# Kernel optimization log

Hardware: AMD Instinct MI355X
Metric: run time of the kernel (lower is better)

## Reference

```python
import jax, jax.numpy as jnp
from jax import lax
import numpy as np

# Config mirroring CSABlock(embed_dim=128, bs=8, heads=8, img_size=512, depth=2)
E = 128
BATCH = 8
HEADS = 8
RESO = 512 // 8      # 64
DEPTH = 2
SPLIT = 2            # split_size
C = 2 * E            # token dim = 256
C2 = C // 2          # per-branch dim
NH = HEADS // 2      # heads per branch
HID = 4 * C          # mlp hidden (mlp_ratio=4)
EPS = 1e-5


def setup_inputs() -> dict:
    key = jax.random.key(0)
    ks = iter(jax.random.split(key, 24))
    rn = lambda s, sd=0.02: jax.random.normal(next(ks), s, jnp.float32) * sd
    return {
        "x1": jax.random.normal(next(ks), (BATCH, E, RESO, RESO), jnp.float32),
        "x2": jax.random.normal(next(ks), (BATCH, E, RESO, RESO), jnp.float32),
        # conv_embed: Conv2d(C,C,3,1,1) + BatchNorm (eval) + LayerNorm
        "conv_w": rn((C, C, 3, 3)), "conv_b": jnp.zeros((C,), jnp.float32),
        "bn_g": jnp.ones((C,), jnp.float32), "bn_b": jnp.zeros((C,), jnp.float32),
        "bn_m": rn((C,), 0.1), "bn_v": jax.random.uniform(next(ks), (C,), jnp.float32) + 0.5,
        "ln0_g": jnp.ones((C,), jnp.float32), "ln0_b": jnp.zeros((C,), jnp.float32),
        # per-CSWinBlock params, stacked over DEPTH
        "n1_g": jnp.ones((DEPTH, C), jnp.float32), "n1_b": jnp.zeros((DEPTH, C), jnp.float32),
        "qkv_w": rn((DEPTH, C, 3 * C)),                       # Linear(dim, 3*dim, bias=False)
        "lepe_w": rn((DEPTH, 2, C2, 1, 3, 3)),                # depthwise get_v conv per branch
        "lepe_b": jnp.zeros((DEPTH, 2, C2), jnp.float32),
        "proj_w": rn((DEPTH, C, C)), "proj_b": jnp.zeros((DEPTH, C), jnp.float32),
        "n2_g": jnp.ones((DEPTH, C), jnp.float32), "n2_b": jnp.zeros((DEPTH, C), jnp.float32),
        "fc1_w": rn((DEPTH, C, HID)), "fc1_b": jnp.zeros((DEPTH, HID), jnp.float32),
        "fc2_w": rn((DEPTH, HID, C)), "fc2_b": jnp.zeros((DEPTH, C), jnp.float32),
    }


def _ln(x, g, b):
    mu = jnp.mean(x, -1, keepdims=True)
    var = jnp.mean((x - mu) ** 2, -1, keepdims=True)
    return (x - mu) * lax.rsqrt(var + EPS) * g + b


def _branch(q, k, v, Hs, Ws, dw_w, dw_b):
    """LePEAttention: cross-shaped stripe window attention with locally-enhanced PE.
    q,k,v: (B, L, C2); stripes of size Hs x Ws over a RESO x RESO grid."""
    B, L, c2 = q.shape
    H = W = RESO
    hd = c2 // NH
    scale = hd ** -0.5

    def to_win(t):  # (B,L,c2) -> (B*nW, NH, Hs*Ws, hd)
        t = t.reshape(B, H // Hs, Hs, W // Ws, Ws, c2)
        t = t.transpose(0, 1, 3, 2, 4, 5).reshape(-1, Hs * Ws, NH, hd)
        return t.transpose(0, 2, 1, 3)

    qw, kw = to_win(q), to_win(k)
    # v as per-window images for the depthwise LePE conv (padding is per-window)
    vimg = v.reshape(B, H // Hs, Hs, W // Ws, Ws, c2).transpose(0, 1, 3, 5, 2, 4)
    vimg = vimg.reshape(-1, c2, Hs, Ws)
    lepe = lax.conv_general_dilated(vimg, dw_w, (1, 1), [(1, 1), (1, 1)],
                                    dimension_numbers=("NCHW", "OIHW", "NCHW"),
                                    feature_group_count=c2) + dw_b[:, None, None]
    heads = lambda t: t.reshape(-1, NH, hd, Hs * Ws).transpose(0, 1, 3, 2)
    vw, lepe = heads(vimg), heads(lepe)

    attn = jax.nn.softmax(jnp.einsum("wnsd,wntd->wnst", qw * scale, kw), axis=-1)
    o = jnp.einsum("wnst,wntd->wnsd", attn, vw) + lepe      # (B*nW, NH, S, hd)
    # windows2img
    o = o.transpose(0, 2, 1, 3).reshape(B, H // Hs, W // Ws, Hs, Ws, c2)
    o = o.transpose(0, 1, 3, 2, 4, 5).reshape(B, L, c2)
    return o


def _forward(x1, x2, conv_w, conv_b, bn_g, bn_b, bn_m, bn_v, ln0_g, ln0_b,
             n1_g, n1_b, qkv_w, lepe_w, lepe_b, proj_w, proj_b,
             n2_g, n2_b, fc1_w, fc1_b, fc2_w, fc2_b):
    B, _, H, W = x1.shape
    t = jnp.concatenate([x1, x2], 1)                                   # (B, C, H, W)
    t = lax.conv_general_dilated(t, conv_w, (1, 1), [(1, 1), (1, 1)],
                                 dimension_numbers=("NCHW", "OIHW", "NCHW")) + conv_b[:, None, None]
    # BatchNorm2d in eval mode (running stats)
    t = (t - bn_m[:, None, None]) * lax.rsqrt(bn_v + EPS)[:, None, None] * bn_g[:, None, None] + bn_b[:, None, None]
    t = t.reshape(B, C, H * W).transpose(0, 2, 1)                      # b c h w -> b (h w) c
    t = _ln(t, ln0_g, ln0_b)

    for i in range(DEPTH):  # CSWinBlock x DEPTH
        img = _ln(t, n1_g[i], n1_b[i])
        qkv = (img @ qkv_w[i]).reshape(B, -1, 3, C)
        q, k, v = qkv[..., 0, :], qkv[..., 1, :], qkv[..., 2, :]
        # branch 0: horizontal stripes (H_sp=RESO, W_sp=SPLIT); branch 1: vertical
        xa = _branch(q[..., :C2], k[..., :C2], v[..., :C2], RESO, SPLIT, lepe_w[i, 0], lepe_b[i, 0])
        xb = _branch(q[..., C2:], k[..., C2:], v[..., C2:], SPLIT, RESO, lepe_w[i, 1], lepe_b[i, 1])
        att = jnp.concatenate([xa, xb], -1) @ proj_w[i] + proj_b[i]
        t = t + att
        y = _ln(t, n2_g[i], n2_b[i])
        t = t + (jax.nn.gelu(y @ fc1_w[i] + fc1_b[i], approximate=False) @ fc2_w[i] + fc2_b[i])

    x = t.transpose(0, 2, 1).reshape(B, C, H, W)
    return x[:, :E], x[:, E:]


def reference(x1, x2, conv_w, conv_b, bn_g, bn_b, bn_m, bn_v, ln0_g, ln0_b,
              n1_g, n1_b, qkv_w, lepe_w, lepe_b, proj_w, proj_b,
              n2_g, n2_b, fc1_w, fc1_b, fc2_w, fc2_b):
    return _forward(x1, x2, conv_w, conv_b, bn_g, bn_b, bn_m, bn_v, ln0_g, ln0_b,
                    n1_g, n1_b, qkv_w, lepe_w, lepe_b, proj_w, proj_b,
                    n2_g, n2_b, fc1_w, fc1_b, fc2_w, fc2_b)
```

## Files before the change

### kernel.cpp

```cpp
#include <hip/hip_runtime.h>
#include <hip/hip_bf16.h>

#define EPSV 1e-5f

using s8v = __attribute__((ext_vector_type(8))) short;
using f4v = __attribute__((ext_vector_type(4))) float;

__device__ __forceinline__ float bf2f(ushort u){
  union { unsigned int i; float f; } x; x.i = ((unsigned int)u)<<16; return x.f;
}
__device__ __forceinline__ ushort f2bf(float f){
  union { float f; unsigned int i; } x; x.f = f;
  unsigned int r = x.i + 0x7FFFu + ((x.i>>16)&1u);
  return (ushort)(r>>16);
}
__device__ __forceinline__ float wsum(float s){
  #pragma unroll
  for (int m=1;m<64;m<<=1) s += __shfl_xor(s, m);
  return s;
}

__device__ __forceinline__ void gload16(const void* g, void* l){
  __builtin_amdgcn_global_load_lds((__attribute__((address_space(1))) void*)g,
                                   (__attribute__((address_space(3))) void*)l, 16, 0, 0);
}

__global__ __launch_bounds__(256) void repack_in_k(const float* __restrict__ x1,
                                                   const float* __restrict__ x2,
                                                   ushort* __restrict__ Xin){
  __shared__ ushort tile[256][66];
  const int y = blockIdx.x, b = blockIdx.y, tid = threadIdx.x;
  const int xl = tid & 63, cq = tid >> 6;
  for (int it=0; it<64; it++){
    int ci = it*4 + cq;
    float v;
    if (ci < 128) v = x1[(((long)b*128 + ci)*64 + y)*64 + xl];
    else          v = x2[(((long)b*128 + (ci-128))*64 + y)*64 + xl];
    tile[ci][xl] = f2bf(v);
  }
  __syncthreads();
  for (int x=0; x<64; x++){
    Xin[(((long)b*66 + (y+1))*66 + (x+1))*256 + tid] = tile[tid][x];
  }
}

__global__ void repack_convw_k(const float* __restrict__ w, ushort* __restrict__ Wc){
  const long total = 256L*2304;
  for (long e = (long)blockIdx.x*blockDim.x + threadIdx.x; e < total; e += (long)gridDim.x*blockDim.x){
    int co = (int)(e / 2304), kk = (int)(e % 2304);
    int dd = kk >> 8, ci = kk & 255;
    Wc[e] = f2bf(w[((long)(co*256 + ci))*9 + dd]);
  }
}

__global__ void transpose_w_k(const float* __restrict__ src, ushort* __restrict__ dst, int K, int N){
  long total = (long)K*N;
  for (long e = (long)blockIdx.x*blockDim.x + threadIdx.x; e < total; e += (long)gridDim.x*blockDim.x){
    int k = (int)(e / N), n = (int)(e % N);
    dst[(long)n*K + k] = f2bf(src[e]);
  }
}

__global__ void bnprep_k(const float* cb, const float* g, const float* b,
                         const float* m, const float* v, float* sc, float* sh){
  int n = threadIdx.x;
  if (n < 256){
    float s = g[n] * rsqrtf(v[n] + EPSV);
    sc[n] = s;
    sh[n] = (cb[n] - m[n])*s + b[n];
  }
}

template<int EPI>
__global__ __launch_bounds__(256) void gemm_f(
    const ushort* __restrict__ A, const ushort* __restrict__ Xin,
    const ushort* __restrict__ Wt, const float* __restrict__ bias,
    const float* __restrict__ sc, const float* __restrict__ sh,
    float* __restrict__ T, const float* __restrict__ g1, const float* __restrict__ b1,
    const float* __restrict__ g2, const float* __restrict__ b2,
    ushort* __restrict__ Xb, float* __restrict__ dout, int K)
{
  constexpr bool CONVA = (EPI==0);
  __shared__ ushort SMEM[40960];
  const int tid = threadIdx.x, wid = tid>>6, lane = tid&63;
  const int m0 = blockIdx.x*64;
  const int l15 = lane&15, lg = lane>>4;
  const int rS = wid*8 + (lane>>3);
  const int cS = (((lane&7) ^ (lane>>3))*8);

  const ushort* pA[2];
  if (CONVA){
    #pragma unroll
    for (int j=0;j<2;j++){
      int t = m0 + j*32 + rS;
      int b = t>>12, y = (t>>6)&63, x = t&63;
      pA[j] = Xin + ((long)((b*66 + y+1)*66) + (x+1))*256 + cS;
    }
  } else {
    #pragma unroll
    for (int j=0;j<2;j++) pA[j] = A + (long)(m0 + j*32 + rS)*K + cS;
  }
  const ushort* pB[8];
  #pragma unroll
  for (int j=0;j<8;j++) pB[j] = Wt + (long)(j*32 + rS)*K + cS;

  auto stage = [&](int buf, int k0){
    ushort* AsB = SMEM + buf*20480;
    ushort* BsB = AsB + 4096;
    int koffA;
    if (CONVA){
      int dd = k0 >> 8;
      int dy = dd/3, dx = dd - dy*3;
      koffA = ((dy-1)*66 + (dx-1))*256 + (k0 & 255);
    } else koffA = k0;
    #pragma unroll
    for (int j=0;j<2;j++)
      gload16(pA[j] + koffA, (void*)&AsB[(j*256 + wid*64)*8]);
    #pragma unroll
    for (int j=0;j<8;j++)
      gload16(pB[j] + k0, (void*)&BsB[(j*256 + wid*64)*8]);
  };

  f4v acc[4][4] = {};

  int cur = 0;
  stage(0, 0);
  __syncthreads();
  for (int k0=0; k0<K; k0+=64){
    if (k0 + 64 < K) stage(cur^1, k0 + 64);
    const ushort* AsB = SMEM + cur*20480;
    const ushort* BsB = AsB + 4096;
    #pragma unroll
    for (int kk=0; kk<2; kk++){
      s8v a[4], b[4];
      const int kch = ((kk*4 + lg) ^ (l15 & 7))*8;
      #pragma unroll
      for (int mi=0;mi<4;mi++) a[mi] = *(const s8v*)&AsB[(mi*16 + l15)*64 + kch];
      #pragma unroll
      for (int ni=0;ni<4;ni++) b[ni] = *(const s8v*)&BsB[(wid*64 + ni*16 + l15)*64 + kch];
      #pragma unroll
      for (int mi=0;mi<4;mi++)
        #pragma unroll
        for (int ni=0;ni<4;ni++)
          acc[mi][ni] = __builtin_amdgcn_mfma_f32_16x16x32_bf16(a[mi], b[ni], acc[mi][ni], 0,0,0);
    }
    __syncthreads();
    cur ^= 1;
  }

  float* CT = (float*)SMEM;
  #pragma unroll
  for (int mi=0;mi<4;mi++)
    #pragma unroll
    for (int ni=0;ni<4;ni++)
      #pragma unroll
      for (int r=0;r<4;r++)
        CT[(mi*16 + lg*4 + r)*256 + wid*64 + ni*16 + l15] = acc[mi][ni][r];
  __syncthreads();

  const int c0 = lane*4;
  float4 scv4, shv4, bias4, g1v, b1v, g2v, b2v;
  if (EPI==0){
    scv4 = *(const float4*)&sc[c0]; shv4 = *(const float4*)&sh[c0];
    g1v = *(const float4*)&g1[c0];  b1v = *(const float4*)&b1[c0];
    g2v = *(const float4*)&g2[c0];  b2v = *(const float4*)&b2[c0];
  } else {
    bias4 = *(const float4*)&bias[c0];
    if (EPI==1){ g1v = *(const float4*)&g1[c0]; b1v = *(const float4*)&b1[c0]; }
  }

  for (int t=0; t<16; t++){
    const int r = wid*16 + t;
    const long gmr = m0 + r;
    float4 v = *(float4*)&CT[r*256 + c0];
    float4 t4;
    if (EPI==0){
      t4.x = v.x*scv4.x + shv4.x; t4.y = v.y*scv4.y + shv4.y;
      t4.z = v.z*scv4.z + shv4.z; t4.w = v.w*scv4.w + shv4.w;
    } else {
      float4 rv = *(float4*)&T[gmr*256 + c0];
      t4.x = rv.x + v.x + bias4.x; t4.y = rv.y + v.y + bias4.y;
      t4.z = rv.z + v.z + bias4.z; t4.w = rv.w + v.w + bias4.w;
    }
    if (EPI==3){
      *(float4*)&CT[r*256 + c0] = t4;
    } else {
      float mu = wsum(t4.x+t4.y+t4.z+t4.w) * (1.0f/256.0f);
      float d0=t4.x-mu, d1=t4.y-mu, d2=t4.z-mu, d3=t4.w-mu;
      float rs = rsqrtf(wsum(d0*d0+d1*d1+d2*d2+d3*d3)*(1.0f/256.0f) + EPSV);
      if (EPI==0){
        float u0 = d0*rs*g1v.x + b1v.x, u1 = d1*rs*g1v.y + b1v.y;
        float u2 = d2*rs*g1v.z + b1v.z, u3 = d3*rs*g1v.w + b1v.w;
        float4 u = {u0,u1,u2,u3};
        *(float4*)&T[gmr*256 + c0] = u;
        float mu2 = wsum(u0+u1+u2+u3) * (1.0f/256.0f);
        float e0=u0-mu2, e1=u1-mu2, e2=u2-mu2, e3=u3-mu2;
        float rs2 = rsqrtf(wsum(e0*e0+e1*e1+e2*e2+e3*e3)*(1.0f/256.0f) + EPSV);
        ushort4 o; o.x=f2bf(e0*rs2*g2v.x + b2v.x); o.y=f2bf(e1*rs2*g2v.y + b2v.y);
        o.z=f2bf(e2*rs2*g2v.z + b2v.z); o.w=f2bf(e3*rs2*g2v.w + b2v.w);
        *(ushort4*)&Xb[gmr*256 + c0] = o;
      } else {
        *(float4*)&T[gmr*256 + c0] = t4;
        ushort4 o; o.x=f2bf(d0*rs*g1v.x + b1v.x); o.y=f2bf(d1*rs*g1v.y + b1v.y);
        o.z=f2bf(d2*rs*g1v.z + b1v.z); o.w=f2bf(d3*rs*g1v.w + b1v.w);
        *(ushort4*)&Xb[gmr*256 + c0] = o;
      }
    }
  }

  if (EPI==3){
    __syncthreads();
    const int b_ = m0>>12, y_ = (m0>>6)&63;
    float* obase = dout + (long)b_*524288 + (long)y_*64;
    for (int it=0; it<64; it++){
      int e = it*256 + tid;
      int c = e>>6, x = e&63;
      obase[(long)(c>>7)*4194304 + (long)(c&127)*4096 + x] = CT[x*256 + c];
    }
  }
}

#define BM 128
#define BN 128
#define BK 64
template<int EPI>
__global__ __launch_bounds__(256) void gemm_k(
    const ushort* __restrict__ A,
    const ushort* __restrict__ Wt, const float* __restrict__ bias,
    ushort* __restrict__ outb, int N, int K)
{
  __shared__ ushort SMEM[BM*BK + BN*BK];
  ushort* As = SMEM;
  ushort* Bs = SMEM + BM*BK;
  const int tid = threadIdx.x, wid = tid>>6, lane = tid&63;
  const int m0 = blockIdx.x*BM, n0 = blockIdx.y*BN;
  const int wm = (wid>>1)*64, wn = (wid&1)*64;
  const int l15 = lane&15, lg = lane>>4;

  const int rA = wid*32 + (lane>>3);
  const int cS = (((lane&7) ^ (lane>>3))*8);
  const ushort* pA[4];
  #pragma unroll
  for (int j=0;j<4;j++) pA[j] = A + (long)(m0 + rA + j*8)*K + cS;
  const ushort* pB[4];
  #pragma unroll
  for (int j=0;j<4;j++) pB[j] = Wt + (long)(n0 + rA + j*8)*K + cS;

  f4v acc[4][4] = {};

  for (int k0=0; k0<K; k0+=BK){
    #pragma unroll
    for (int j=0;j<4;j++){
      gload16(pA[j] + k0, (void*)&As[(wid*32 + j*8)*BK]);
      gload16(pB[j] + k0, (void*)&Bs[(wid*32 + j*8)*BK]);
    }
    __syncthreads();
    #pragma unroll
    for (int kk=0; kk<2; kk++){
      s8v a[4], b[4];
      const int kch = ((kk*4 + lg) ^ (l15 & 7))*8;
      #pragma unroll
      for (int mi=0;mi<4;mi++) a[mi] = *(const s8v*)&As[(wm + mi*16 + l15)*BK + kch];
      #pragma unroll
      for (int ni=0;ni<4;ni++) b[ni] = *(const s8v*)&Bs[(wn + ni*16 + l15)*BK + kch];
      #pragma unroll
      for (int mi=0;mi<4;mi++)
        #pragma unroll
        for (int ni=0;ni<4;ni++)
          acc[mi][ni] = __builtin_amdgcn_mfma_f32_16x16x32_bf16(a[mi], b[ni], acc[mi][ni], 0,0,0);
    }
    __syncthreads();
  }

  if (EPI == 4){
    #pragma unroll
    for (int mi=0;mi<4;mi++)
      #pragma unroll
      for (int ni=0;ni<4;ni++)
        #pragma unroll
        for (int r=0;r<4;r++){
          int gm = m0 + wm + mi*16 + lg*4 + r;
          int gn = n0 + wn + ni*16 + l15;
          float v = acc[mi][ni][r];
          int tile = gn >> 8;
          int c = gn & 255;
          int br2 = (c >> 7) & 1;
          int hh = (c >> 5) & 3;
          int d = c & 31;
          int bb2 = gm >> 12;
          int y = (gm >> 6) & 63;
          int x = gm & 63;
          int wv, sv;
          if (br2 == 0){ wv = x >> 1; sv = (y << 1) | (x & 1); }
          else         { wv = y >> 1; sv = ((y & 1) << 6) | x; }
          long row = ((long)bb2*32 + wv)*128 + sv;
          outb[(((long)(tile*2 + br2)*4 + hh)*32768L + row)*32 + d] = f2bf(v);
        }
  } else {
    float* CT = (float*)SMEM;
    #pragma unroll
    for (int p=0; p<2; p++){
      if ((wid>>1) == p){
        #pragma unroll
        for (int mi=0;mi<4;mi++)
          #pragma unroll
          for (int ni=0;ni<4;ni++)
            #pragma unroll
            for (int r=0;r<4;r++)
              CT[(mi*16 + lg*4 + r)*128 + wn + ni*16 + l15] = acc[mi][ni][r];
      }
      __syncthreads();
      #pragma unroll
      for (int it=0; it<8; it++){
        int e = it*256 + tid;
        int row = e >> 5;
        int c4 = e & 31;
        float4 v = *(float4*)&CT[row*128 + c4*4];
        int gm = m0 + p*64 + row;
        int gn = n0 + c4*4;
        float4 bv = *(const float4*)&bias[gn];
        float t0 = v.x + bv.x, t1 = v.y + bv.y, t2 = v.z + bv.z, t3 = v.w + bv.w;
        t0 = 0.5f*t0*(1.0f + erff(t0*0.70710678118654752f));
        t1 = 0.5f*t1*(1.0f + erff(t1*0.70710678118654752f));
        t2 = 0.5f*t2*(1.0f + erff(t2*0.70710678118654752f));
        t3 = 0.5f*t3*(1.0f + erff(t3*0.70710678118654752f));
        ushort4 u; u.x=f2bf(t0); u.y=f2bf(t1); u.z=f2bf(t2); u.w=f2bf(t3);
        *(ushort4*)&outb[(long)gm*N + gn] = u;
      }
      __syncthreads();
    }
  }
}

template<int BR>
__global__ __launch_bounds__(256) void attn_k(
    const ushort* __restrict__ QKVw, ushort* __restrict__ ATT,
    const float* __restrict__ lepe_w, const float* __restrict__ lepe_b, int layer)
{
  __shared__ ushort q_lds[128][36];
  __shared__ ushort k_lds[128][36];
  __shared__ ushort vT[32][132];
  __shared__ float wl[32][9];
  __shared__ float bl[32];
  const int tid = threadIdx.x, wid = tid>>6, lane = tid&63;
  const int b = blockIdx.y;
  const int w = blockIdx.x>>2, h = blockIdx.x&3;
  const int choff = BR*128 + h*32;
  const int l15 = lane&15, lg = lane>>4;

  const long rowbase = ((long)b*32 + w)*128;
  const ushort* qb = QKVw + (((long)(0*2+BR)*4 + h)*32768L + rowbase)*32;
  const ushort* kb = QKVw + (((long)(1*2+BR)*4 + h)*32768L + rowbase)*32;
  const ushort* vb = QKVw + (((long)(2*2+BR)*4 + h)*32768L + rowbase)*32;

  for (int e = tid; e < 512; e += 256){
    int row = e>>2, c4 = (e&3)*8;
    *(uint4*)&q_lds[row][c4] = *(const uint4*)(qb + (long)e*8);
    *(uint4*)&k_lds[row][c4] = *(const uint4*)(kb + (long)e*8);
    uint4 val = *(const uint4*)(vb + (long)e*8);
    const ushort* u = (const ushort*)&val;
    #pragma unroll
    for (int jj=0;jj<8;jj++) vT[c4+jj][row] = u[jj];
  }
  for (int e = tid; e < 288; e += 256){
    int d = e/9, tap = e%9;
    wl[d][tap] = lepe_w[((long)((layer*2+BR)*128 + h*32 + d))*9 + tap];
  }
  if (tid < 32) bl[tid] = lepe_b[(layer*2+BR)*128 + h*32 + tid];
  __syncthreads();

  const int wrow = wid*32;
  const float scale = 0.17677669529663689f;
  const int srcE = (lane & 15) | ((lane & 16) << 1);
  const int srcO = srcE + 16;
  const bool hi = (lane >= 32);

  #pragma unroll
  for (int mi=0; mi<2; mi++){
    s8v aq = *(const s8v*)&q_lds[wrow + mi*16 + l15][lg*8];
    f4v S[8];
    #pragma unroll
    for (int ni=0; ni<8; ni++){
      s8v bk = *(const s8v*)&k_lds[ni*16 + l15][lg*8];
      f4v z = {0.f,0.f,0.f,0.f};
      S[ni] = __builtin_amdgcn_mfma_f32_16x16x32_bf16(bk, aq, z, 0,0,0);
    }
    float mx = -1e30f;
    #pragma unroll
    for (int ni=0; ni<8; ni++)
      #pragma unroll
      for (int r=0;r<4;r++){ S[ni][r] *= scale; mx = fmaxf(mx, S[ni][r]); }
    mx = fmaxf(mx, __shfl_xor(mx, 16));
    mx = fmaxf(mx, __shfl_xor(mx, 32));
    float sum = 0.f;
    #pragma unroll
    for (int ni=0; ni<8; ni++)
      #pragma unroll
      for (int r=0;r<4;r++){ S[ni][r] = __expf(S[ni][r]-mx); sum += S[ni][r]; }
    sum += __shfl_xor(sum, 16);
    sum += __shfl_xor(sum, 32);
    const float inv = 1.0f / sum;
    unsigned int Alo[8], Ahi[8];
    #pragma unroll
    for (int ni=0; ni<8; ni++){
      Alo[ni] = (unsigned)f2bf(S[ni][0]*inv) | ((unsigned)f2bf(S[ni][1]*inv)<<16);
      Ahi[ni] = (unsigned)f2bf(S[ni][2]*inv) | ((unsigned)f2bf(S[ni][3]*inv)<<16);
    }
    f4v acc2[2] = {{0.f,0.f,0.f,0.f},{0.f,0.f,0.f,0.f}};
    #pragma unroll
    for (int ks=0; ks<4; ks++){
      unsigned e0 = (unsigned)__shfl((int)Alo[2*ks],   srcE);
      unsigned e1 = (unsigned)__shfl((int)Ahi[2*ks],   srcE);
      unsigned e2 = (unsigned)__shfl((int)Alo[2*ks+1], srcE);
      unsigned e3 = (unsigned)__shfl((int)Ahi[2*ks+1], srcE);
      unsigned o0 = (unsigned)__shfl((int)Alo[2*ks],   srcO);
      unsigned o1 = (unsigned)__shfl((int)Ahi[2*ks],   srcO);
      unsigned o2 = (unsigned)__shfl((int)Alo[2*ks+1], srcO);
      unsigned o3 = (unsigned)__shfl((int)Ahi[2*ks+1], srcO);
      union { unsigned u[4]; s8v v; } ap;
      ap.u[0] = hi?e2:e0; ap.u[1] = hi?e3:e1; ap.u[2] = hi?o2:o0; ap.u[3] = hi?o3:o1;
      #pragma unroll
      for (int di=0; di<2; di++){
        s8v bv = *(const s8v*)&vT[di*16 + l15][ks*32 + lg*8];
        acc2[di] = __builtin_amdgcn_mfma_f32_16x16x32_bf16(ap.v, bv, acc2[di], 0,0,0);
      }
    }
    #pragma unroll
    for (int di=0; di<2; di++)
      #pragma unroll
      for (int r=0;r<4;r++){
        int s = wrow + mi*16 + lg*4 + r;
        int d = di*16 + l15;
        float v = acc2[di][r] + bl[d];
        const int HsL = (BR==0)?64:2, WsL = (BR==0)?2:64;
        int hs, ws2;
        if (BR==0){ hs = s>>1; ws2 = s&1; }
        else      { hs = s>>6; ws2 = s&63; }
        #pragma unroll
        for (int a=-1;a<=1;a++)
          #pragma unroll
          for (int bb=-1;bb<=1;bb++){
            int h2 = hs+a, w2 = ws2+bb;
            if (h2>=0 && h2<HsL && w2>=0 && w2<WsL){
              int s2 = h2*WsL + w2;
              v += wl[d][(a+1)*3 + (bb+1)] * bf2f(vT[d][s2]);
            }
          }
        int y, x;
        if (BR==0){ y = s>>1; x = (w<<1)|(s&1); }
        else      { y = (w<<1)|(s>>6); x = s&63; }
        long tok = ((long)b*64 + y)*64 + x;
        ATT[tok*256 + choff + d] = f2bf(v);
      }
  }
}

extern "C" void kernel_launch(void* const* d_in, const int* in_sizes, int n_in,
                              void* d_out, int out_size, void* d_ws, size_t ws_size,
                              hipStream_t stream)
{
  (void)in_sizes; (void)n_in; (void)out_size;
  const float* x1     = (const float*)d_in[0];
  const float* x2     = (const float*)d_in[1];
  const float* conv_w = (const float*)d_in[2];
  const float* conv_b = (const float*)d_in[3];
  const float* bn_g   = (const float*)d_in[4];
  const float* bn_b   = (const float*)d_in[5];
  const float* bn_m   = (const float*)d_in[6];
  const float* bn_v   = (const float*)d_in[7];
  const float* ln0_g  = (const float*)d_in[8];
  const float* ln0_b  = (const float*)d_in[9];
  const float* n1_g   = (const float*)d_in[10];
  const float* n1_b   = (const float*)d_in[11];
  const float* qkv_w  = (const float*)d_in[12];
  const float* lepe_w = (const float*)d_in[13];
  const float* lepe_b = (const float*)d_in[14];
  const float* proj_w = (const float*)d_in[15];
  const float* proj_b = (const float*)d_in[16];
  const float* n2_g   = (const float*)d_in[17];
  const float* n2_b   = (const float*)d_in[18];
  const float* fc1_w  = (const float*)d_in[19];
  const float* fc1_b  = (const float*)d_in[20];
  const float* fc2_w  = (const float*)d_in[21];
  const float* fc2_b  = (const float*)d_in[22];

  if (ws_size < 121767936ULL){
    hipMemsetAsync(d_out, 0, (size_t)out_size*4, stream);
    return;
  }

  char* ws = (char*)d_ws;
  ushort* Xin  = (ushort*)ws;
  ushort* QKVb = (ushort*)ws;
  ushort* H1b  = (ushort*)ws;
  ushort* ATTb = (ushort*)(ws + 50331648);
  float*  T    = (float*)(ws + 67108864);
  ushort* Xb   = (ushort*)(ws + 100663296);
  size_t off = 117440512;
  ushort* Wc   = (ushort*)(ws + off); off += 1179648;
  ushort* Wq   = (ushort*)(ws + off); off += 786432;
  ushort* Wp   = (ushort*)(ws + off); off += 262144;
  ushort* W1   = (ushort*)(ws + off); off += 1048576;
  ushort* W2   = (ushort*)(ws + off); off += 1048576;
  float*  scv  = (float*)(ws + off);  off += 1024;
  float*  shv  = (float*)(ws + off);  off += 1024;

  hipMemsetAsync(Xin, 0, (size_t)8*66*66*256*2, stream);
  repack_in_k<<<dim3(64,8), 256, 0, stream>>>(x1, x2, Xin);
  repack_convw_k<<<576, 256, 0, stream>>>(conv_w, Wc);
  for (int i=0;i<2;i++){
    transpose_w_k<<<512,256,0,stream>>>(qkv_w + (long)i*196608, Wq + (long)i*196608, 256, 768);
    transpose_w_k<<<128,256,0,stream>>>(proj_w + (long)i*65536, Wp + (long)i*65536, 256, 256);
    transpose_w_k<<<512,256,0,stream>>>(fc1_w + (long)i*262144, W1 + (long)i*262144, 256, 1024);
    transpose_w_k<<<512,256,0,stream>>>(fc2_w + (long)i*262144, W2 + (long)i*262144, 1024, 256);
  }
  bnprep_k<<<1,256,0,stream>>>(conv_b, bn_g, bn_b, bn_m, bn_v, scv, shv);

  gemm_f<0><<<512,256,0,stream>>>(nullptr, Xin, Wc, nullptr, scv, shv,
                                  T, ln0_g, ln0_b, n1_g, n1_b, Xb, nullptr, 2304);

  for (int i=0;i<2;i++){
    gemm_k<4><<<dim3(256,6),256,0,stream>>>(Xb, Wq + (long)i*196608, nullptr, QKVb, 768, 256);
    attn_k<0><<<dim3(128,8),256,0,stream>>>(QKVb, ATTb, lepe_w, lepe_b, i);
    attn_k<1><<<dim3(128,8),256,0,stream>>>(QKVb, ATTb, lepe_w, lepe_b, i);
    gemm_f<1><<<512,256,0,stream>>>(ATTb, nullptr, Wp + (long)i*65536, proj_b + i*256,
                                    nullptr, nullptr, T, n2_g + i*256, n2_b + i*256,
                                    nullptr, nullptr, Xb, nullptr, 256);
    gemm_k<1><<<dim3(256,8),256,0,stream>>>(Xb, W1 + (long)i*262144, fc1_b + i*1024, H1b, 1024, 256);
    if (i == 0){
      gemm_f<1><<<512,256,0,stream>>>(H1b, nullptr, W2, fc2_b,
                                      nullptr, nullptr, T, n1_g + 256, n1_b + 256,
                                      nullptr, nullptr, Xb, nullptr, 1024);
    } else {
      gemm_f<3><<<512,256,0,stream>>>(H1b, nullptr, W2 + 262144, fc2_b + 256,
                                      nullptr, nullptr, T, nullptr, nullptr,
                                      nullptr, nullptr, nullptr, (float*)d_out, 1024);
    }
  }
}
```

Before: 486.5 us.

## Fuse MLP fc1, GELU and fc2 into one kernel; stage QKV epilogue through LDS

Adds an mlp_f kernel. Each block computes a 64-row fc1 tile in chunks of 256 hidden units, applies bias and GELU, and keeps the bf16 hidden tile in swizzled LDS. It then accumulates fc2 directly and finishes with the residual add and LayerNorm or the final output transpose. This removes the global write and re-read of the 1024-wide hidden activation each layer, at the cost of re-streaming both weight matrices per block from L2. It also uses more LDS per block and has no double buffering. Separately, the QKV GEMM epilogue now stages bf16 results in swizzled LDS and writes coalesced 16-byte segments into the stripe layout, replacing scattered per-element stores.

Measured after the change: 549.3 us. 1.13x slower.

```diff
diff --git a/kernel.cpp b/kernel.cpp
--- a/kernel.cpp
+++ b/kernel.cpp
@@ -18,6 +18,9 @@
   #pragma unroll
   for (int m=1;m<64;m<<=1) s += __shfl_xor(s, m);
   return s;
+}
+__device__ __forceinline__ float gelu_f(float t){
+  return 0.5f*t*(1.0f + erff(t*0.70710678118654752f));
 }
 
 __device__ __forceinline__ void gload16(const void* g, void* l){
@@ -166,7 +169,7 @@
     g2v = *(const float4*)&g2[c0];  b2v = *(const float4*)&b2[c0];
   } else {
     bias4 = *(const float4*)&bias[c0];
-    if (EPI==1){ g1v = *(const float4*)&g1[c0]; b1v = *(const float4*)&b1[c0]; }
+    g1v = *(const float4*)&g1[c0]; b1v = *(const float4*)&b1[c0];
   }
 
   for (int t=0; t<16; t++){
@@ -182,29 +185,149 @@
       t4.x = rv.x + v.x + bias4.x; t4.y = rv.y + v.y + bias4.y;
       t4.z = rv.z + v.z + bias4.z; t4.w = rv.w + v.w + bias4.w;
     }
+    float mu = wsum(t4.x+t4.y+t4.z+t4.w) * (1.0f/256.0f);
+    float d0=t4.x-mu, d1=t4.y-mu, d2=t4.z-mu, d3=t4.w-mu;
+    float rs = rsqrtf(wsum(d0*d0+d1*d1+d2*d2+d3*d3)*(1.0f/256.0f) + EPSV);
+    if (EPI==0){
+      float u0 = d0*rs*g1v.x + b1v.x, u1 = d1*rs*g1v.y + b1v.y;
+      float u2 = d2*rs*g1v.z + b1v.z, u3 = d3*rs*g1v.w + b1v.w;
+      float4 u = {u0,u1,u2,u3};
+      *(float4*)&T[gmr*256 + c0] = u;
+      float mu2 = wsum(u0+u1+u2+u3) * (1.0f/256.0f);
+      float e0=u0-mu2, e1=u1-mu2, e2=u2-mu2, e3=u3-mu2;
+      float rs2 = rsqrtf(wsum(e0*e0+e1*e1+e2*e2+e3*e3)*(1.0f/256.0f) + EPSV);
+      ushort4 o; o.x=f2bf(e0*rs2*g2v.x + b2v.x); o.y=f2bf(e1*rs2*g2v.y + b2v.y);
+      o.z=f2bf(e2*rs2*g2v.z + b2v.z); o.w=f2bf(e3*rs2*g2v.w + b2v.w);
+      *(ushort4*)&Xb[gmr*256 + c0] = o;
+    } else {
+      *(float4*)&T[gmr*256 + c0] = t4;
+      ushort4 o; o.x=f2bf(d0*rs*g1v.x + b1v.x); o.y=f2bf(d1*rs*g1v.y + b1v.y);
+      o.z=f2bf(d2*rs*g1v.z + b1v.z); o.w=f2bf(d3*rs*g1v.w + b1v.w);
+      *(ushort4*)&Xb[gmr*256 + c0] = o;
+    }
+  }
+}
+
+template<int EPI>
+__global__ __launch_bounds__(256) void mlp_f(
+    const ushort* __restrict__ Xb, const ushort* __restrict__ W1t, const float* __restrict__ w1b,
+    const ushort* __restrict__ W2t, const float* __restrict__ w2b,
+    float* __restrict__ T, const float* __restrict__ lng, const float* __restrict__ lnb,
+    ushort* __restrict__ XbOut, float* __restrict__ dout)
+{
+  __shared__ ushort SMEM[36864];
+  ushort* As = SMEM;
+  ushort* Bs = SMEM + 4096;
+  ushort* H  = SMEM + 20480;
+  const int tid = threadIdx.x, wid = tid>>6, lane = tid&63;
+  const int m0 = blockIdx.x*64;
+  const int l15 = lane&15, lg = lane>>4;
+  const int rS = wid*8 + (lane>>3);
+  const int cS = (((lane&7) ^ (lane>>3))*8);
+
+  const ushort* pA[2];
+  #pragma unroll
+  for (int j=0;j<2;j++) pA[j] = Xb + (long)(m0 + j*32 + rS)*256 + cS;
+
+  f4v acc2[4][4] = {};
+
+  for (int hc=0; hc<4; hc++){
+    f4v acc1[4][4] = {};
+    for (int ks=0; ks<4; ks++){
+      const int k0 = ks*64;
+      #pragma unroll
+      for (int j=0;j<2;j++)
+        gload16(pA[j] + k0, (void*)&As[(j*256 + wid*64)*8]);
+      #pragma unroll
+      for (int j=0;j<8;j++)
+        gload16(W1t + (long)(hc*256 + j*32 + rS)*256 + k0 + cS, (void*)&Bs[(j*256 + wid*64)*8]);
+      __syncthreads();
+      #pragma unroll
+      for (int kk=0; kk<2; kk++){
+        s8v a[4], b[4];
+        const int kch = ((kk*4 + lg) ^ (l15 & 7))*8;
+        #pragma unroll
+        for (int mi=0;mi<4;mi++) a[mi] = *(const s8v*)&As[(mi*16 + l15)*64 + kch];
+        #pragma unroll
+        for (int ni=0;ni<4;ni++) b[ni] = *(const s8v*)&Bs[(wid*64 + ni*16 + l15)*64 + kch];
+        #pragma unroll
+        for (int mi=0;mi<4;mi++)
+          #pragma unroll
+          for (int ni=0;ni<4;ni++)
+            acc1[mi][ni] = __builtin_amdgcn_mfma_f32_16x16x32_bf16(a[mi], b[ni], acc1[mi][ni], 0,0,0);
+      }
+      __syncthreads();
+    }
+    #pragma unroll
+    for (int ni=0;ni<4;ni++){
+      const int c = wid*64 + ni*16 + l15;
+      const float bv = w1b[hc*256 + c];
+      const int j = c>>3, ce = c&7;
+      #pragma unroll
+      for (int mi=0;mi<4;mi++)
+        #pragma unroll
+        for (int r=0;r<4;r++){
+          const int row = mi*16 + lg*4 + r;
+          H[row*256 + (((j ^ (row&7))<<3) | ce)] = f2bf(gelu_f(acc1[mi][ni][r] + bv));
+        }
+    }
+    for (int ks2=0; ks2<4; ks2++){
+      #pragma unroll
+      for (int j=0;j<8;j++)
+        gload16(W2t + (long)(j*32 + rS)*1024 + hc*256 + ks2*64 + cS, (void*)&Bs[(j*256 + wid*64)*8]);
+      __syncthreads();
+      #pragma unroll
+      for (int kk=0; kk<2; kk++){
+        s8v a[4], b[4];
+        const int kch = ((kk*4 + lg) ^ (l15 & 7))*8;
+        #pragma unroll
+        for (int mi=0;mi<4;mi++)
+          a[mi] = *(const s8v*)&H[(mi*16 + l15)*256 + (((ks2*8 + kk*4 + lg) ^ (l15&7))*8)];
+        #pragma unroll
+        for (int ni=0;ni<4;ni++) b[ni] = *(const s8v*)&Bs[(wid*64 + ni*16 + l15)*64 + kch];
+        #pragma unroll
+        for (int mi=0;mi<4;mi++)
+          #pragma unroll
+          for (int ni=0;ni<4;ni++)
+            acc2[mi][ni] = __builtin_amdgcn_mfma_f32_16x16x32_bf16(a[mi], b[ni], acc2[mi][ni], 0,0,0);
+      }
+      __syncthreads();
+    }
+  }
+
+  float* CT = (float*)SMEM;
+  #pragma unroll
+  for (int mi=0;mi<4;mi++)
+    #pragma unroll
+    for (int ni=0;ni<4;ni++)
+      #pragma unroll
+      for (int r=0;r<4;r++)
+        CT[(mi*16 + lg*4 + r)*256 + wid*64 + ni*16 + l15] = acc2[mi][ni][r];
+  __syncthreads();
+
+  const int c0 = lane*4;
+  const float4 bias4 = *(const float4*)&w2b[c0];
+  float4 g1v, b1v;
+  if (EPI==1){ g1v = *(const float4*)&lng[c0]; b1v = *(const float4*)&lnb[c0]; }
+
+  for (int t=0; t<16; t++){
+    const int r = wid*16 + t;
+    const long gmr = m0 + r;
+    float4 v = *(float4*)&CT[r*256 + c0];
+    float4 rv = *(float4*)&T[gmr*256 + c0];
+    float4 t4;
+    t4.x = rv.x + v.x + bias4.x; t4.y = rv.y + v.y + bias4.y;
+    t4.z = rv.z + v.z + bias4.z; t4.w = rv.w + v.w + bias4.w;
     if (EPI==3){
       *(float4*)&CT[r*256 + c0] = t4;
     } else {
+      *(float4*)&T[gmr*256 + c0] = t4;
       float mu = wsum(t4.x+t4.y+t4.z+t4.w) * (1.0f/256.0f);
       float d0=t4.x-mu, d1=t4.y-mu, d2=t4.z-mu, d3=t4.w-mu;
       float rs = rsqrtf(wsum(d0*d0+d1*d1+d2*d2+d3*d3)*(1.0f/256.0f) + EPSV);
-      if (EPI==0){
-        float u0 = d0*rs*g1v.x + b1v.x, u1 = d1*rs*g1v.y + b1v.y;
-        float u2 = d2*rs*g1v.z + b1v.z, u3 = d3*rs*g1v.w + b1v.w;
-        float4 u = {u0,u1,u2,u3};
-        *(float4*)&T[gmr*256 + c0] = u;
-        float mu2 = wsum(u0+u1+u2+u3) * (1.0f/256.0f);
-        float e0=u0-mu2, e1=u1-mu2, e2=u2-mu2, e3=u3-mu2;
-        float rs2 = rsqrtf(wsum(e0*e0+e1*e1+e2*e2+e3*e3)*(1.0f/256.0f) + EPSV);
-        ushort4 o; o.x=f2bf(e0*rs2*g2v.x + b2v.x); o.y=f2bf(e1*rs2*g2v.y + b2v.y);
-        o.z=f2bf(e2*rs2*g2v.z + b2v.z); o.w=f2bf(e3*rs2*g2v.w + b2v.w);
-        *(ushort4*)&Xb[gmr*256 + c0] = o;
-      } else {
-        *(float4*)&T[gmr*256 + c0] = t4;
-        ushort4 o; o.x=f2bf(d0*rs*g1v.x + b1v.x); o.y=f2bf(d1*rs*g1v.y + b1v.y);
-        o.z=f2bf(d2*rs*g1v.z + b1v.z); o.w=f2bf(d3*rs*g1v.w + b1v.w);
-        *(ushort4*)&Xb[gmr*256 + c0] = o;
-      }
+      ushort4 o; o.x=f2bf(d0*rs*g1v.x + b1v.x); o.y=f2bf(d1*rs*g1v.y + b1v.y);
+      o.z=f2bf(d2*rs*g1v.z + b1v.z); o.w=f2bf(d3*rs*g1v.w + b1v.w);
+      *(ushort4*)&XbOut[gmr*256 + c0] = o;
     }
   }
 
@@ -223,11 +346,10 @@
 #define BM 128
 #define BN 128
 #define BK 64
-template<int EPI>
-__global__ __launch_bounds__(256) void gemm_k(
+__global__ __launch_bounds__(256) void gemm_qkv(
     const ushort* __restrict__ A,
-    const ushort* __restrict__ Wt, const float* __restrict__ bias,
-    ushort* __restrict__ outb, int N, int K)
+    const ushort* __restrict__ Wt,
+    ushort* __restrict__ outb, int K)
 {
   __shared__ ushort SMEM[BM*BK + BN*BK];
   ushort* As = SMEM;
@@ -272,62 +394,48 @@
     __syncthreads();
   }
 
-  if (EPI == 4){
+  ushort* CB = SMEM;
+  #pragma unroll
+  for (int ni=0;ni<4;ni++){
+    const int c = wn + ni*16 + l15;
+    const int j = c>>3, ce = c&7;
     #pragma unroll
     for (int mi=0;mi<4;mi++)
       #pragma unroll
-      for (int ni=0;ni<4;ni++)
-        #pragma unroll
-        for (int r=0;r<4;r++){
-          int gm = m0 + wm + mi*16 + lg*4 + r;
-          int gn = n0 + wn + ni*16 + l15;
-          float v = acc[mi][ni][r];
-          int tile = gn >> 8;
-          int c = gn & 255;
-          int br2 = (c >> 7) & 1;
-          int hh = (c >> 5) & 3;
-          int d = c & 31;
-          int bb2 = gm >> 12;
-          int y = (gm >> 6) & 63;
-          int x = gm & 63;
-          int wv, sv;
-          if (br2 == 0){ wv = x >> 1; sv = (y << 1) | (x & 1); }
-          else         { wv = y >> 1; sv = ((y & 1) << 6) | x; }
-          long row = ((long)bb2*32 + wv)*128 + sv;
-          outb[(((long)(tile*2 + br2)*4 + hh)*32768L + row)*32 + d] = f2bf(v);
-        }
+      for (int r=0;r<4;r++){
+        const int row = wm + mi*16 + lg*4 + r;
+        CB[row*128 + (((j ^ (row&7))<<3) | ce)] = f2bf(acc[mi][ni][r]);
+      }
+  }
+  __syncthreads();
+
+  const int tile = n0 >> 8;
+  const int brq  = (n0 >> 7) & 1;
+  const int b_   = m0 >> 12;
+  const int Y0   = (m0 >> 6) & 63;
+  if (brq == 0){
+    #pragma unroll
+    for (int it=0; it<8; it++){
+      int g = it*256 + tid;
+      int seg = g >> 4, q = g & 15;
+      int h = seg >> 5, wv = seg & 31;
+      int svi = q >> 2, c8 = q & 3;
+      int gm_local = (svi>>1)*64 + wv*2 + (svi&1);
+      int jc = h*4 + c8;
+      uint4 v = *(uint4*)&CB[gm_local*128 + ((jc ^ (gm_local&7))<<3)];
+      long rowb = ((long)(tile*2)*4 + h)*32768L + ((long)b_*32 + wv)*128 + (Y0*2 + svi);
+      *(uint4*)&outb[rowb*32 + c8*8] = v;
+    }
   } else {
-    float* CT = (float*)SMEM;
-    #pragma unroll
-    for (int p=0; p<2; p++){
-      if ((wid>>1) == p){
-        #pragma unroll
-        for (int mi=0;mi<4;mi++)
-          #pragma unroll
-          for (int ni=0;ni<4;ni++)
-            #pragma unroll
-            for (int r=0;r<4;r++)
-              CT[(mi*16 + lg*4 + r)*128 + wn + ni*16 + l15] = acc[mi][ni][r];
-      }
-      __syncthreads();
-      #pragma unroll
-      for (int it=0; it<8; it++){
-        int e = it*256 + tid;
-        int row = e >> 5;
-        int c4 = e & 31;
-        float4 v = *(float4*)&CT[row*128 + c4*4];
-        int gm = m0 + p*64 + row;
-        int gn = n0 + c4*4;
-        float4 bv = *(const float4*)&bias[gn];
-        float t0 = v.x + bv.x, t1 = v.y + bv.y, t2 = v.z + bv.z, t3 = v.w + bv.w;
-        t0 = 0.5f*t0*(1.0f + erff(t0*0.70710678118654752f));
-        t1 = 0.5f*t1*(1.0f + erff(t1*0.70710678118654752f));
-        t2 = 0.5f*t2*(1.0f + erff(t2*0.70710678118654752f));
-        t3 = 0.5f*t3*(1.0f + erff(t3*0.70710678118654752f));
-        ushort4 u; u.x=f2bf(t0); u.y=f2bf(t1); u.z=f2bf(t2); u.w=f2bf(t3);
-        *(ushort4*)&outb[(long)gm*N + gn] = u;
-      }
-      __syncthreads();
+    const int wv = Y0 >> 1;
+    #pragma unroll
+    for (int it=0; it<8; it++){
+      int g = it*256 + tid;
+      int h = g >> 9, rem = g & 511, sv = rem >> 2, c8 = rem & 3;
+      int jc = h*4 + c8;
+      uint4 v = *(uint4*)&CB[sv*128 + ((jc ^ (sv&7))<<3)];
+      long rowb = ((long)(tile*2 + 1)*4 + h)*32768L + ((long)b_*32 + wv)*128 + sv;
+      *(uint4*)&outb[rowb*32 + c8*8] = v;
     }
   }
 }
@@ -490,12 +598,12 @@
   }
 
   char* ws = (char*)d_ws;
-  ushort* Xin  = (ushort*)ws;
-  ushort* QKVb = (ushort*)ws;
-  ushort* H1b  = (ushort*)ws;
-  ushort* ATTb = (ushort*)(ws + 50331648);
-  float*  T    = (float*)(ws + 67108864);
-  ushort* Xb   = (ushort*)(ws + 100663296);
+  ushort* Xin    = (ushort*)ws;
+  ushort* QKVb   = (ushort*)ws;
+  ushort* ATTb   = (ushort*)(ws + 50331648);
+  ushort* XbNext = (ushort*)(ws + 50331648);
+  float*  T      = (float*)(ws + 67108864);
+  ushort* XbA    = (ushort*)(ws + 100663296);
   size_t off = 117440512;
   ushort* Wc   = (ushort*)(ws + off); off += 1179648;
   ushort* Wq   = (ushort*)(ws + off); off += 786432;
@@ -517,24 +625,23 @@
   bnprep_k<<<1,256,0,stream>>>(conv_b, bn_g, bn_b, bn_m, bn_v, scv, shv);
 
   gemm_f<0><<<512,256,0,stream>>>(nullptr, Xin, Wc, nullptr, scv, shv,
-                                  T, ln0_g, ln0_b, n1_g, n1_b, Xb, nullptr, 2304);
-
-  for (int i=0;i<2;i++){
-    gemm_k<4><<<dim3(256,6),256,0,stream>>>(Xb, Wq + (long)i*196608, nullptr, QKVb, 768, 256);
-    attn_k<0><<<dim3(128,8),256,0,stream>>>(QKVb, ATTb, lepe_w, lepe_b, i);
-    attn_k<1><<<dim3(128,8),256,0,stream>>>(QKVb, ATTb, lepe_w, lepe_b, i);
-    gemm_f<1><<<512,256,0,stream>>>(ATTb, nullptr, Wp + (long)i*65536, proj_b + i*256,
-                                    nullptr, nullptr, T, n2_g + i*256, n2_b + i*256,
-                                    nullptr, nullptr, Xb, nullptr, 256);
-    gemm_k<1><<<dim3(256,8),256,0,stream>>>(Xb, W1 + (long)i*262144, fc1_b + i*1024, H1b, 1024, 256);
-    if (i == 0){
-      gemm_f<1><<<512,256,0,stream>>>(H1b, nullptr, W2, fc2_b,
-                                      nullptr, nullptr, T, n1_g + 256, n1_b + 256,
-                                      nullptr, nullptr, Xb, nullptr, 1024);
-    } else {
-      gemm_f<3><<<512,256,0,stream>>>(H1b, nullptr, W2 + 262144, fc2_b + 256,
-                                      nullptr, nullptr, T, nullptr, nullptr,
-                                      nullptr, nullptr, nullptr, (float*)d_out, 1024);
-    }
-  }
-}
+                                  T, ln0_g, ln0_b, n1_g, n1_b, XbA, nullptr, 2304);
+
+  gemm_qkv<<<dim3(256,6),256,0,stream>>>(XbA, Wq, QKVb, 256);
+  attn_k<0><<<dim3(128,8),256,0,stream>>>(QKVb, ATTb, lepe_w, lepe_b, 0);
+  attn_k<1><<<dim3(128,8),256,0,stream>>>(QKVb, ATTb, lepe_w, lepe_b, 0);
+  gemm_f<1><<<512,256,0,stream>>>(ATTb, nullptr, Wp, proj_b,
+                                  nullptr, nullptr, T, n2_g, n2_b,
+                                  nullptr, nullptr, XbA, nullptr, 256);
+  mlp_f<1><<<512,256,0,stream>>>(XbA, W1, fc1_b, W2, fc2_b,
+                                 T, n1_g + 256, n1_b + 256, XbNext, nullptr);
+
+  gemm_qkv<<<dim3(256,6),256,0,stream>>>(XbNext, Wq + 196608, QKVb, 256);
+  attn_k<0><<<dim3(128,8),256,0,stream>>>(QKVb, ATTb, lepe_w, lepe_b, 1);
+  attn_k<1><<<dim3(128,8),256,0,stream>>>(QKVb, ATTb, lepe_w, lepe_b, 1);
+  gemm_f<1><<<512,256,0,stream>>>(ATTb, nullptr, Wp + 65536, proj_b + 256,
+                                  nullptr, nullptr, T, n2_g + 256, n2_b + 256,
+                                  nullptr, nullptr, XbA, nullptr, 256);
+  mlp_f<3><<<512,256,0,stream>>>(XbA, W1 + 262144, fc1_b + 1024, W2 + 262144, fc2_b + 256,
+                                 T, nullptr, nullptr, nullptr, (float*)d_out);
+}
```
